# Kernel tuning notes

Measured on AMD Instinct MI355X. Metric: run time of the kernel, lower is better.

## Reference

```python
import jax, jax.numpy as jnp
import numpy as np

N, E = 50000, 1600000
IN_DIM, EMBED, OUT = 512, 128, 64


def setup_inputs() -> dict:
    key = jax.random.key(0)
    k = jax.random.split(key, 8)
    x = jax.random.normal(k[0], (N, IN_DIM), dtype=jnp.float32)
    edge_index = jax.random.randint(k[1], (2, E), 0, N, dtype=jnp.int32)
    W_dense = jax.random.normal(k[2], (EMBED, IN_DIM), dtype=jnp.float32) * 0.02
    b_dense = jnp.zeros((EMBED,), dtype=jnp.float32)
    W_gat = jax.random.normal(k[3], (OUT, EMBED), dtype=jnp.float32) * 0.05
    att_src = jax.random.normal(k[4], (OUT,), dtype=jnp.float32) * 0.1
    att_dst = jax.random.normal(k[5], (OUT,), dtype=jnp.float32) * 0.1
    b_gat = jnp.zeros((OUT,), dtype=jnp.float32)
    return {"x": x, "edge_index": edge_index, "W_dense": W_dense, "b_dense": b_dense,
            "W_gat": W_gat, "att_src": att_src, "att_dst": att_dst, "b_gat": b_gat}


def reference(x, edge_index, W_dense, b_dense, W_gat, att_src, att_dst, b_gat):
    # dense -> LeakyReLU(0.01) (nn.LeakyReLU default)
    h = jax.nn.leaky_relu(x @ W_dense.T + b_dense, negative_slope=0.01)  # [N, EMBED]
    n = h.shape[0]
    # GATConv (PyG, heads=1, add_self_loops=True, negative_slope=0.2)
    loops = jnp.arange(n, dtype=edge_index.dtype)
    src = jnp.concatenate([edge_index[0], loops])
    dst = jnp.concatenate([edge_index[1], loops])
    g = h @ W_gat.T  # [N, OUT]
    a_src = g @ att_src  # [N]
    a_dst = g @ att_dst  # [N]
    e = jax.nn.leaky_relu(a_src[src] + a_dst[dst], negative_slope=0.2)  # [E+N]
    # segment softmax over destination neighborhoods (self loops guarantee non-empty)
    m = jax.ops.segment_max(e, dst, num_segments=n)
    e = jnp.exp(e - m[dst])
    denom = jax.ops.segment_sum(e, dst, num_segments=n)
    alpha = e / denom[dst]
    out = jax.ops.segment_sum(g[src] * alpha[:, None], dst, num_segments=n) + b_gat
    # original returns ([embed_x], [embed_x]); we return the single embedding tensor
    return out
```

## Files before the change

kernel.cpp:

```cpp
#include <hip/hip_runtime.h>
#include <math.h>

#define IN_DIM 512
#define EMBED 128
#define OUT_DIM 64
#define NBPAD 256
#define SEGSH 12
#define CAP_LDS 10240

typedef __attribute__((ext_vector_type(8))) short bf16x8;
typedef __attribute__((ext_vector_type(4))) float f32x4;

__device__ __forceinline__ float lrelu(float v, float s) { return v > 0.f ? v : v * s; }

__device__ __forceinline__ float readlane_f(float v, int l) {
  return __int_as_float(__builtin_amdgcn_readlane(__float_as_int(v), l));
}

__device__ __forceinline__ unsigned short f2bf(float f) {
  unsigned int u = __float_as_uint(f);
  u += 0x7fff + ((u >> 16) & 1);
  return (unsigned short)(u >> 16);
}
__device__ __forceinline__ float bf2f(unsigned short h) {
  return __uint_as_float(((unsigned int)h) << 16);
}

__device__ __forceinline__ unsigned int cvt_pk_bf16(float a, float b) {
  unsigned int r;
  asm("v_cvt_pk_bf16_f32 %0, %1, %2" : "=v"(r) : "v"(a), "v"(b));
  return r;
}

__device__ __forceinline__ void gl_lds16(const void* g, void* l) {
  __builtin_amdgcn_global_load_lds(
      (const __attribute__((address_space(1))) unsigned int*)g,
      (__attribute__((address_space(3))) unsigned int*)l, 16, 0, 0);
}

#define LDA 40

__global__ __launch_bounds__(256) void split_w_kernel(
    const float* __restrict__ Wd, unsigned short* __restrict__ Wdh,
    unsigned short* __restrict__ Wdl, const float* __restrict__ Wg,
    unsigned short* __restrict__ Wgh, unsigned short* __restrict__ Wgl) {
  int i = (blockIdx.x * 256 + threadIdx.x) * 4;
  const float* W;
  unsigned short *Wh, *Wl;
  int base;
  if (i < EMBED * IN_DIM) {
    W = Wd; Wh = Wdh; Wl = Wdl; base = i;
  } else {
    base = i - EMBED * IN_DIM;
    if (base >= OUT_DIM * EMBED) return;
    W = Wg; Wh = Wgh; Wl = Wgl;
  }
  float4 v = *(const float4*)(W + base);
  unsigned int h0 = cvt_pk_bf16(v.x, v.y);
  unsigned int h1 = cvt_pk_bf16(v.z, v.w);
  float r0 = v.x - __uint_as_float(h0 << 16);
  float r1 = v.y - __uint_as_float(h0 & 0xffff0000u);
  float r2 = v.z - __uint_as_float(h1 << 16);
  float r3 = v.w - __uint_as_float(h1 & 0xffff0000u);
  unsigned int l0 = cvt_pk_bf16(r0, r1);
  unsigned int l1 = cvt_pk_bf16(r2, r3);
  *(uint2*)(Wh + base) = make_uint2(h0, h1);
  *(uint2*)(Wl + base) = make_uint2(l0, l1);
}

__global__ __launch_bounds__(256) void gemm1_mfma_kernel(
    const float* __restrict__ x, const unsigned short* __restrict__ Wdh,
    const unsigned short* __restrict__ Wdl, const float* __restrict__ bd,
    unsigned int* __restrict__ hp, int N) {
  __shared__ __align__(16) unsigned char Bhs[2][8192];
  __shared__ __align__(16) unsigned char Bls[2][8192];

  const int tid = threadIdx.x;
  const int lane = tid & 63;
  const int wid = tid >> 6;
  const int mblk = blockIdx.x * 128;
  const int quad = lane >> 4;
  const int l15 = lane & 15;

  const float* aptr[2];
#pragma unroll
  for (int mi = 0; mi < 2; ++mi) {
    int rg = mblk + wid * 32 + mi * 16 + l15;
    if (rg >= N) rg = N - 1;
    aptr[mi] = x + (size_t)rg * IN_DIM + quad * 8;
  }
  float4 tc[2][2];
  auto loadA = [&](int k0) {
#pragma unroll
    for (int mi = 0; mi < 2; ++mi) {
      tc[mi][0] = *(const float4*)(aptr[mi] + k0);
      tc[mi][1] = *(const float4*)(aptr[mi] + k0 + 4);
    }
  };

  const char* bsrcH[2];
  const char* bsrcL[2];
  int bdst[2];
#pragma unroll
  for (int i = 0; i < 2; ++i) {
    int chunk = i * 256 + tid;
    int row = chunk >> 2, ch = chunk & 3;
    int cs = ch ^ ((row >> 1) & 3);
    size_t srcoff = (size_t)row * (IN_DIM * 2) + (cs << 4);
    bsrcH[i] = (const char*)Wdh + srcoff;
    bsrcL[i] = (const char*)Wdl + srcoff;
    bdst[i] = chunk * 16;
  }
  auto stageB = [&](int buf, int k0) {
    const size_t kb = (size_t)k0 * 2;
#pragma unroll
    for (int i = 0; i < 2; ++i) {
      gl_lds16(bsrcH[i] + kb, Bhs[buf] + bdst[i]);
      gl_lds16(bsrcL[i] + kb, Bls[buf] + bdst[i]);
    }
  };

  int boff[8];
#pragma unroll
  for (int ni = 0; ni < 8; ++ni) {
    int row = ni * 16 + l15;
    boff[ni] = row * 64 + ((quad ^ ((row >> 1) & 3)) << 4);
  }

  f32x4 acc[2][8];
#pragma unroll
  for (int i = 0; i < 2; ++i)
#pragma unroll
    for (int j = 0; j < 8; ++j) acc[i][j] = (f32x4){0.f, 0.f, 0.f, 0.f};

  stageB(0, 0);
  loadA(0);
  __syncthreads();

#pragma unroll 2
  for (int s = 0; s < IN_DIM / 32; ++s) {
    const int buf = s & 1;
    if (s + 1 < IN_DIM / 32) stageB(buf ^ 1, (s + 1) * 32);

    bf16x8 AH[2], AL[2];
#pragma unroll
    for (int mi = 0; mi < 2; ++mi) {
      float av[8] = {tc[mi][0].x, tc[mi][0].y, tc[mi][0].z, tc[mi][0].w,
                     tc[mi][1].x, tc[mi][1].y, tc[mi][1].z, tc[mi][1].w};
      union { unsigned int u[4]; bf16x8 v; } H, L;
#pragma unroll
      for (int i = 0; i < 4; ++i) {
        unsigned int hpk = cvt_pk_bf16(av[2 * i], av[2 * i + 1]);
        float q0 = av[2 * i] - __uint_as_float(hpk << 16);
        float q1 = av[2 * i + 1] - __uint_as_float(hpk & 0xffff0000u);
        H.u[i] = hpk;
        L.u[i] = cvt_pk_bf16(q0, q1);
      }
      AH[mi] = H.v;
      AL[mi] = L.v;
    }
    if (s + 1 < IN_DIM / 32) loadA((s + 1) * 32);

#pragma unroll
    for (int hf = 0; hf < 2; ++hf) {
      bf16x8 BH[4], BL[4];
#pragma unroll
      for (int j = 0; j < 4; ++j) {
        BH[j] = *(const bf16x8*)(Bhs[buf] + boff[hf * 4 + j]);
        BL[j] = *(const bf16x8*)(Bls[buf] + boff[hf * 4 + j]);
      }
#pragma unroll
      for (int mi = 0; mi < 2; ++mi)
#pragma unroll
        for (int j = 0; j < 4; ++j) {
          int ni = hf * 4 + j;
          acc[mi][ni] = __builtin_amdgcn_mfma_f32_16x16x32_bf16(AH[mi], BH[j], acc[mi][ni], 0, 0, 0);
          acc[mi][ni] = __builtin_amdgcn_mfma_f32_16x16x32_bf16(AL[mi], BH[j], acc[mi][ni], 0, 0, 0);
          acc[mi][ni] = __builtin_amdgcn_mfma_f32_16x16x32_bf16(AH[mi], BL[j], acc[mi][ni], 0, 0, 0);
        }
    }
    __syncthreads();
  }

#pragma unroll
  for (int mi = 0; mi < 2; ++mi)
#pragma unroll
    for (int ni = 0; ni < 8; ++ni) {
      int n = ni * 16 + l15;
      float b = bd[n];
#pragma unroll
      for (int r = 0; r < 4; ++r) {
        int m = mblk + wid * 32 + mi * 16 + quad * 4 + r;
        float v = lrelu(acc[mi][ni][r] + b, 0.01f);
        unsigned short hi = f2bf(v);
        unsigned short lo = f2bf(v - bf2f(hi));
        if (m < N) hp[(size_t)m * EMBED + n] = ((unsigned int)hi << 16) | lo;
      }
    }
}

__global__ __launch_bounds__(256) void gemm2_mfma_kernel(
    const unsigned int* __restrict__ hp, const unsigned short* __restrict__ Wgh,
    const unsigned short* __restrict__ Wgl, const float* __restrict__ att_src,
    const float* __restrict__ att_dst, float* __restrict__ g,
    float* __restrict__ a_src, float* __restrict__ a_dst, int N) {
  __shared__ __align__(16) unsigned char Bhs[16384];
  __shared__ __align__(16) unsigned char Bls[16384];

  const int tid = threadIdx.x;
  const int lane = tid & 63;
  const int wid = tid >> 6;
  const int mblk = blockIdx.x * 128;
  const int quad = lane >> 4;
  const int l15 = lane & 15;

  const char* aptr[2];
#pragma unroll
  for (int mi = 0; mi < 2; ++mi) {
    int rg = mblk + wid * 32 + mi * 16 + l15;
    if (rg >= N) rg = N - 1;
    aptr[mi] = (const char*)hp + (size_t)rg * (EMBED * 4) + quad * 32;
  }
  uint4 areg[2][4][2];
#pragma unroll
  for (int mi = 0; mi < 2; ++mi)
#pragma unroll
    for (int ks = 0; ks < 4; ++ks) {
      areg[mi][ks][0] = *(const uint4*)(aptr[mi] + ks * 128);
      areg[mi][ks][1] = *(const uint4*)(aptr[mi] + ks * 128 + 16);
    }

#pragma unroll
  for (int i = 0; i < 4; ++i) {
    int chunk = i * 256 + tid;
    int row = chunk >> 4, ch = chunk & 15;
    size_t srcoff = (size_t)row * (EMBED * 2) + ((ch ^ (row & 15)) << 4);
    gl_lds16((const char*)Wgh + srcoff, Bhs + chunk * 16);
    gl_lds16((const char*)Wgl + srcoff, Bls + chunk * 16);
  }
  __syncthreads();

  f32x4 acc[2][4];
#pragma unroll
  for (int i = 0; i < 2; ++i)
#pragma unroll
    for (int j = 0; j < 4; ++j) acc[i][j] = (f32x4){0.f, 0.f, 0.f, 0.f};

#pragma unroll
  for (int ks = 0; ks < 4; ++ks) {
    bf16x8 AH[2], AL[2];
#pragma unroll
    for (int mi = 0; mi < 2; ++mi) {
      union { unsigned int u[8]; uint4 v[2]; } W_;
      W_.v[0] = areg[mi][ks][0];
      W_.v[1] = areg[mi][ks][1];
      union { unsigned int u[4]; bf16x8 v; } H, L;
#pragma unroll
      for (int p = 0; p < 4; ++p) {
        unsigned int wA = W_.u[2 * p], wB = W_.u[2 * p + 1];
        H.u[p] = __builtin_amdgcn_perm(wB, wA, 0x07060302u);
        L.u[p] = __builtin_amdgcn_perm(wB, wA, 0x05040100u);
      }
      AH[mi] = H.v;
      AL[mi] = L.v;
    }
#pragma unroll
    for (int ni = 0; ni < 4; ++ni) {
      int row = ni * 16 + l15;
      int chunk = ks * 4 + quad;
      int off = row * 256 + (((chunk ^ (row & 15))) << 4);
      bf16x8 BH = *(const bf16x8*)(Bhs + off);
      bf16x8 BL = *(const bf16x8*)(Bls + off);
#pragma unroll
      for (int mi = 0; mi < 2; ++mi) {
        acc[mi][ni] = __builtin_amdgcn_mfma_f32_16x16x32_bf16(AH[mi], BH, acc[mi][ni], 0, 0, 0);
        acc[mi][ni] = __builtin_amdgcn_mfma_f32_16x16x32_bf16(AL[mi], BH, acc[mi][ni], 0, 0, 0);
        acc[mi][ni] = __builtin_amdgcn_mfma_f32_16x16x32_bf16(AH[mi], BL, acc[mi][ni], 0, 0, 0);
      }
    }
  }

  float as_[4], ad_[4];
#pragma unroll
  for (int ni = 0; ni < 4; ++ni) {
    int n = ni * 16 + l15;
    as_[ni] = att_src[n];
    ad_[ni] = att_dst[n];
  }
#pragma unroll
  for (int mi = 0; mi < 2; ++mi) {
#pragma unroll
    for (int r = 0; r < 4; ++r) {
      int m = mblk + wid * 32 + mi * 16 + quad * 4 + r;
      float ps = acc[mi][0][r] * as_[0] + acc[mi][1][r] * as_[1] +
                 acc[mi][2][r] * as_[2] + acc[mi][3][r] * as_[3];
      float pd = acc[mi][0][r] * ad_[0] + acc[mi][1][r] * ad_[1] +
                 acc[mi][2][r] * ad_[2] + acc[mi][3][r] * ad_[3];
#pragma unroll
      for (int d = 1; d < 16; d <<= 1) {
        ps += __shfl_xor(ps, d, 64);
        pd += __shfl_xor(pd, d, 64);
      }
      if (m < N) {
#pragma unroll
        for (int ni = 0; ni < 4; ++ni)
          g[(size_t)m * OUT_DIM + ni * 16 + l15] = acc[mi][ni][r];
        if (l15 == 0) {
          a_src[m] = ps;
          a_dst[m] = pd;
        }
      }
    }
  }
}

__global__ __launch_bounds__(256) void hist_count_kernel(
    const int* __restrict__ ei, int* __restrict__ histT, int nblkP, int E,
    int N) {
  __shared__ int cnt[NBPAD];
  const int t = threadIdx.x;
  cnt[t] = 0;
  __syncthreads();
  const int T = E + N;
  const int base = blockIdx.x << SEGSH;
#pragma unroll
  for (int q = 0; q < (1 << SEGSH) / 256; ++q) {
    int i = base + q * 256 + t;
    if (i < T) {
      int d = (i < E) ? ei[E + i] : (i - E);
      atomicAdd(&cnt[d >> 8], 1);
    }
  }
  __syncthreads();
  histT[(size_t)t * nblkP + blockIdx.x] = cnt[t];
}

__global__ __launch_bounds__(256) void row_scan_kernel(
    int* __restrict__ histT, int* __restrict__ bucket_tot, int nblkP) {
  __shared__ int sc[256];
  const int t = threadIdx.x;
  int* row = histT + (size_t)blockIdx.x * nblkP;
  const int per = (nblkP + 255) / 256;
  int loc[8];
  int sum = 0;
#pragma unroll 4
  for (int j = 0; j < per; ++j) {
    int idx = t * per + j;
    int v = (idx < nblkP) ? row[idx] : 0;
    loc[j] = sum;
    sum += v;
  }
  sc[t] = sum;
  __syncthreads();
  for (int dlt = 1; dlt < 256; dlt <<= 1) {
    int add = (t >= dlt) ? sc[t - dlt] : 0;
    __syncthreads();
    sc[t] += add;
    __syncthreads();
  }
  const int off = sc[t] - sum;
#pragma unroll 4
  for (int j = 0; j < per; ++j) {
    int idx = t * per + j;
    if (idx < nblkP) row[idx] = off + loc[j];
  }
  if (t == 255) bucket_tot[blockIdx.x] = sc[255];
}

__global__ __launch_bounds__(256) void base_scan_kernel(
    const int* __restrict__ bucket_tot, int* __restrict__ bucket_base,
    int* __restrict__ offsets, int N, int T) {
  __shared__ int sc[256];
  const int t = threadIdx.x;
  int v = bucket_tot[t];
  sc[t] = v;
  __syncthreads();
  for (int dlt = 1; dlt < 256; dlt <<= 1) {
    int add = (t >= dlt) ? sc[t - dlt] : 0;
    __syncthreads();
    sc[t] += add;
    __syncthreads();
  }
  bucket_base[t] = sc[t] - v;
  if (t == 0) offsets[N] = T;
}

__global__ __launch_bounds__(256) void bin_kernel(
    const int* __restrict__ ei, const int* __restrict__ histT,
    const int* __restrict__ bucket_base, int* __restrict__ stageB, int nblkP,
    int E, int N) {
  __shared__ int cnt[NBPAD];
  __shared__ int basev[NBPAD];
  const int t = threadIdx.x;
  cnt[t] = 0;
  basev[t] = bucket_base[t] + histT[(size_t)t * nblkP + blockIdx.x];
  __syncthreads();
  const int T = E + N;
  const int base = blockIdx.x << SEGSH;
#pragma unroll
  for (int q = 0; q < (1 << SEGSH) / 256; ++q) {
    int i = base + q * 256 + t;
    if (i < T) {
      int s, d;
      if (i < E) {
        s = ei[i];
        d = ei[E + i];
      } else {
        s = d = i - E;
      }
      int b = d >> 8;
      int r = atomicAdd(&cnt[b], 1);
      stageB[basev[b] + r] = (s << 8) | (d & 255);
    }
  }
}

__global__ __launch_bounds__(256) void build_kernel(
    const int* __restrict__ stageB, const int* __restrict__ bucket_base,
    const int* __restrict__ bucket_tot, const float* __restrict__ a_src,
    const float* __restrict__ a_dst, int* __restrict__ offsets,
    int2* __restrict__ csr_pack, int N) {
  __shared__ int cnt[256];
  __shared__ int pre[256];
  __shared__ int cur[256];
  __shared__ int2 buf[CAP_LDS];
  const int b = blockIdx.x;
  const int t = threadIdx.x;
  const int base = bucket_base[b];
  const int tot = bucket_tot[b];
  cnt[t] = 0;
  __syncthreads();
  const int* sp = stageB + base;
  for (int i = t; i < tot; i += 256) atomicAdd(&cnt[sp[i] & 255], 1);
  __syncthreads();
  int v = cnt[t];
  pre[t] = v;
  __syncthreads();
  for (int dlt = 1; dlt < 256; dlt <<= 1) {
    int add = (t >= dlt) ? pre[t - dlt] : 0;
    __syncthreads();
    pre[t] += add;
    __syncthreads();
  }
  const int excl = pre[t] - v;
  cur[t] = excl;
  const int d_self = (b << 8) | t;
  if (d_self < N) offsets[d_self] = base + excl;
  __syncthreads();
  for (int i = t; i < tot; i += 256) {
    int rec = sp[i];
    int dl = rec & 255;
    int s = rec >> 8;
    float e = a_src[s] + a_dst[(b << 8) | dl];
    e = e > 0.f ? e : 0.2f * e;
    int pos = atomicAdd(&cur[dl], 1);
    int2 r2 = make_int2(s, __float_as_int(e));
    if (pos < CAP_LDS)
      buf[pos] = r2;
    else
      csr_pack[base + pos] = r2;
  }
  __syncthreads();
  const int lim = min(tot, CAP_LDS);
  for (int i = t; i < lim; i += 256) csr_pack[base + i] = buf[i];
}

__global__ __launch_bounds__(256) void aggregate_kernel(
    const int* __restrict__ offsets, const int2* __restrict__ csr_pack,
    const float* __restrict__ g, const float* __restrict__ b_gat,
    float* __restrict__ out, int N) {
  const int lane = threadIdx.x & 63;
  const int node = blockIdx.x * 4 + (threadIdx.x >> 6);
  if (node >= N) return;
  const int beg = offsets[node], end = offsets[node + 1];

  float m = -1e30f;
  for (int j = beg + lane; j < end; j += 64)
    m = fmaxf(m, __int_as_float(csr_pack[j].y));
#pragma unroll
  for (int d = 1; d < 64; d <<= 1) m = fmaxf(m, __shfl_xor(m, d, 64));

  float l = 0.f;
  for (int j = beg + lane; j < end; j += 64)
    l += __expf(__int_as_float(csr_pack[j].y) - m);
#pragma unroll
  for (int d = 1; d < 64; d <<= 1) l += __shfl_xor(l, d, 64);
  const float inv_l = 1.f / l;

  float acc0 = 0.f, acc1 = 0.f, acc2 = 0.f, acc3 = 0.f;
  for (int jb = beg; jb < end; jb += 64) {
    int j = jb + lane;
    float p = 0.f;
    int s = 0;
    if (j < end) {
      int2 rec = csr_pack[j];
      p = __expf(__int_as_float(rec.y) - m) * inv_l;
      s = rec.x;
    }
    const int cnt = min(64, end - jb);
    int jj = 0;
    for (; jj + 4 <= cnt; jj += 4) {
      int s0 = __builtin_amdgcn_readlane(s, jj);
      int s1 = __builtin_amdgcn_readlane(s, jj + 1);
      int s2 = __builtin_amdgcn_readlane(s, jj + 2);
      int s3 = __builtin_amdgcn_readlane(s, jj + 3);
      float p0 = readlane_f(p, jj);
      float p1 = readlane_f(p, jj + 1);
      float p2 = readlane_f(p, jj + 2);
      float p3 = readlane_f(p, jj + 3);
      acc0 += p0 * g[((size_t)s0 << 6) + lane];
      acc1 += p1 * g[((size_t)s1 << 6) + lane];
      acc2 += p2 * g[((size_t)s2 << 6) + lane];
      acc3 += p3 * g[((size_t)s3 << 6) + lane];
    }
    for (; jj < cnt; ++jj) {
      int s0 = __builtin_amdgcn_readlane(s, jj);
      float p0 = readlane_f(p, jj);
      acc0 += p0 * g[((size_t)s0 << 6) + lane];
    }
  }
  out[(size_t)node * OUT_DIM + lane] = (acc0 + acc1) + (acc2 + acc3) + b_gat[lane];
}

extern "C" void kernel_launch(void* const* d_in, const int* in_sizes, int n_in,
                              void* d_out, int out_size, void* d_ws, size_t ws_size,
                              hipStream_t stream) {
  const float* x = (const float*)d_in[0];
  const int* ei = (const int*)d_in[1];
  const float* Wd = (const float*)d_in[2];
  const float* bd = (const float*)d_in[3];
  const float* Wg = (const float*)d_in[4];
  const float* att_src = (const float*)d_in[5];
  const float* att_dst = (const float*)d_in[6];
  const float* bg = (const float*)d_in[7];
  float* out = (float*)d_out;

  const int N = in_sizes[0] / IN_DIM;
  const int E = in_sizes[1] / 2;
  const int T = E + N;
  const int NB = (N + 255) >> 8;
  const int nblkP = (T + (1 << SEGSH) - 1) >> SEGSH;

  char* ws = (char*)d_ws;
  size_t off = 0;
  auto alloc = [&](size_t bytes) -> void* {
    void* p = ws + off;
    off += (bytes + 15) & ~(size_t)15;
    return p;
  };
  unsigned int* hpk = (unsigned int*)alloc((size_t)N * EMBED * 4);
  float* g = (float*)alloc((size_t)N * OUT_DIM * 4);
  float* a_src = (float*)alloc((size_t)N * 4);
  float* a_dst = (float*)alloc((size_t)N * 4);
  int* offsets = (int*)alloc((size_t)(N + 1) * 4);
  int* histT = (int*)alloc((size_t)NBPAD * nblkP * 4);
  int* bucket_base = (int*)alloc((size_t)NBPAD * 4);
  int* bucket_tot = (int*)alloc((size_t)NBPAD * 4);
  int* stageB = (int*)alloc((size_t)T * 4);
  int2* csr_pack = (int2*)alloc((size_t)T * 8);
  unsigned short* Wdh = (unsigned short*)alloc((size_t)EMBED * IN_DIM * 2);
  unsigned short* Wdl = (unsigned short*)alloc((size_t)EMBED * IN_DIM * 2);
  unsigned short* Wgh = (unsigned short*)alloc((size_t)OUT_DIM * EMBED * 2);
  unsigned short* Wgl = (unsigned short*)alloc((size_t)OUT_DIM * EMBED * 2);

  const int SPLIT_TOT = EMBED * IN_DIM + OUT_DIM * EMBED;
  hipLaunchKernelGGL(split_w_kernel, dim3(SPLIT_TOT / 1024), dim3(256), 0,
                     stream, Wd, Wdh, Wdl, Wg, Wgh, Wgl);
  hipLaunchKernelGGL(gemm1_mfma_kernel, dim3((N + 127) / 128), dim3(256), 0,
                     stream, x, Wdh, Wdl, bd, hpk, N);
  hipLaunchKernelGGL(gemm2_mfma_kernel, dim3((N + 127) / 128), dim3(256), 0,
                     stream, hpk, Wgh, Wgl, att_src, att_dst, g, a_src, a_dst, N);
  hipLaunchKernelGGL(hist_count_kernel, dim3(nblkP), dim3(256), 0, stream,
                     ei, histT, nblkP, E, N);
  hipLaunchKernelGGL(row_scan_kernel, dim3(NBPAD), dim3(256), 0, stream,
                     histT, bucket_tot, nblkP);
  hipLaunchKernelGGL(base_scan_kernel, dim3(1), dim3(256), 0, stream,
                     bucket_tot, bucket_base, offsets, N, T);
  hipLaunchKernelGGL(bin_kernel, dim3(nblkP), dim3(256), 0, stream,
                     ei, histT, bucket_base, stageB, nblkP, E, N);
  hipLaunchKernelGGL(build_kernel, dim3(NB), dim3(256), 0, stream,
                     stageB, bucket_base, bucket_tot, a_src, a_dst, offsets,
                     csr_pack, N);
  hipLaunchKernelGGL(aggregate_kernel, dim3((N + 3) / 4), dim3(256), 0, stream,
                     offsets, csr_pack, g, bg, out, N);
}
```

Measured before the change: 316.6 us.

## Use 512-thread blocks in gemm1 and single-pass online softmax in aggregate

The first GEMM now runs 8 waves per block, each handling 16 rows instead of 32. This halves per-thread accumulators and A registers, and spreads the B staging over more threads, for more latency hiding and occupancy. The aggregate kernel merges the max pass and the sum-of-exp pass into one online-softmax pass with a combined (max, sum) wave reduction, so csr_pack is read one time fewer. The cost is extra exp calls in the loop and reduction, and less MFMA work per wave to amortise each LDS read of B.

```diff
diff --git a/kernel.cpp b/kernel.cpp
--- a/kernel.cpp
+++ b/kernel.cpp
@@ -37,8 +37,6 @@
       (const __attribute__((address_space(1))) unsigned int*)g,
       (__attribute__((address_space(3))) unsigned int*)l, 16, 0, 0);
 }
-
-#define LDA 40
 
 __global__ __launch_bounds__(256) void split_w_kernel(
     const float* __restrict__ Wd, unsigned short* __restrict__ Wdh,
@@ -68,7 +66,7 @@
   *(uint2*)(Wl + base) = make_uint2(l0, l1);
 }
 
-__global__ __launch_bounds__(256) void gemm1_mfma_kernel(
+__global__ __launch_bounds__(512) void gemm1_mfma_kernel(
     const float* __restrict__ x, const unsigned short* __restrict__ Wdh,
     const unsigned short* __restrict__ Wdl, const float* __restrict__ bd,
     unsigned int* __restrict__ hp, int N) {
@@ -82,42 +80,31 @@
   const int quad = lane >> 4;
   const int l15 = lane & 15;
 
-  const float* aptr[2];
-#pragma unroll
-  for (int mi = 0; mi < 2; ++mi) {
-    int rg = mblk + wid * 32 + mi * 16 + l15;
-    if (rg >= N) rg = N - 1;
-    aptr[mi] = x + (size_t)rg * IN_DIM + quad * 8;
-  }
-  float4 tc[2][2];
+  int rg = mblk + wid * 16 + l15;
+  if (rg >= N) rg = N - 1;
+  const float* aptr = x + (size_t)rg * IN_DIM + quad * 8;
+  float4 tc0, tc1;
   auto loadA = [&](int k0) {
-#pragma unroll
-    for (int mi = 0; mi < 2; ++mi) {
-      tc[mi][0] = *(const float4*)(aptr[mi] + k0);
-      tc[mi][1] = *(const float4*)(aptr[mi] + k0 + 4);
-    }
+    tc0 = *(const float4*)(aptr + k0);
+    tc1 = *(const float4*)(aptr + k0 + 4);
   };
 
-  const char* bsrcH[2];
-  const char* bsrcL[2];
-  int bdst[2];
-#pragma unroll
-  for (int i = 0; i < 2; ++i) {
-    int chunk = i * 256 + tid;
+  const char* bsrcH;
+  const char* bsrcL;
+  int bdstv;
+  {
+    int chunk = tid;
     int row = chunk >> 2, ch = chunk & 3;
     int cs = ch ^ ((row >> 1) & 3);
     size_t srcoff = (size_t)row * (IN_DIM * 2) + (cs << 4);
-    bsrcH[i] = (const char*)Wdh + srcoff;
-    bsrcL[i] = (const char*)Wdl + srcoff;
-    bdst[i] = chunk * 16;
+    bsrcH = (const char*)Wdh + srcoff;
+    bsrcL = (const char*)Wdl + srcoff;
+    bdstv = chunk * 16;
   }
   auto stageB = [&](int buf, int k0) {
     const size_t kb = (size_t)k0 * 2;
-#pragma unroll
-    for (int i = 0; i < 2; ++i) {
-      gl_lds16(bsrcH[i] + kb, Bhs[buf] + bdst[i]);
-      gl_lds16(bsrcL[i] + kb, Bls[buf] + bdst[i]);
-    }
+    gl_lds16(bsrcH + kb, Bhs[buf] + bdstv);
+    gl_lds16(bsrcL + kb, Bls[buf] + bdstv);
   };
 
   int boff[8];
@@ -127,11 +114,9 @@
     boff[ni] = row * 64 + ((quad ^ ((row >> 1) & 3)) << 4);
   }
 
-  f32x4 acc[2][8];
-#pragma unroll
-  for (int i = 0; i < 2; ++i)
-#pragma unroll
-    for (int j = 0; j < 8; ++j) acc[i][j] = (f32x4){0.f, 0.f, 0.f, 0.f};
+  f32x4 acc[8];
+#pragma unroll
+  for (int j = 0; j < 8; ++j) acc[j] = (f32x4){0.f, 0.f, 0.f, 0.f};
 
   stageB(0, 0);
   loadA(0);
@@ -142,11 +127,9 @@
     const int buf = s & 1;
     if (s + 1 < IN_DIM / 32) stageB(buf ^ 1, (s + 1) * 32);
 
-    bf16x8 AH[2], AL[2];
-#pragma unroll
-    for (int mi = 0; mi < 2; ++mi) {
-      float av[8] = {tc[mi][0].x, tc[mi][0].y, tc[mi][0].z, tc[mi][0].w,
-                     tc[mi][1].x, tc[mi][1].y, tc[mi][1].z, tc[mi][1].w};
+    bf16x8 AH, AL;
+    {
+      float av[8] = {tc0.x, tc0.y, tc0.z, tc0.w, tc1.x, tc1.y, tc1.z, tc1.w};
       union { unsigned int u[4]; bf16x8 v; } H, L;
 #pragma unroll
       for (int i = 0; i < 4; ++i) {
@@ -156,8 +139,8 @@
         H.u[i] = hpk;
         L.u[i] = cvt_pk_bf16(q0, q1);
       }
-      AH[mi] = H.v;
-      AL[mi] = L.v;
+      AH = H.v;
+      AL = L.v;
     }
     if (s + 1 < IN_DIM / 32) loadA((s + 1) * 32);
 
@@ -170,33 +153,29 @@
         BL[j] = *(const bf16x8*)(Bls[buf] + boff[hf * 4 + j]);
       }
 #pragma unroll
-      for (int mi = 0; mi < 2; ++mi)
-#pragma unroll
-        for (int j = 0; j < 4; ++j) {
-          int ni = hf * 4 + j;
-          acc[mi][ni] = __builtin_amdgcn_mfma_f32_16x16x32_bf16(AH[mi], BH[j], acc[mi][ni], 0, 0, 0);
-          acc[mi][ni] = __builtin_amdgcn_mfma_f32_16x16x32_bf16(AL[mi], BH[j], acc[mi][ni], 0, 0, 0);
-          acc[mi][ni] = __builtin_amdgcn_mfma_f32_16x16x32_bf16(AH[mi], BL[j], acc[mi][ni], 0, 0, 0);
-        }
-    }
-    __syncthreads();
-  }
-
-#pragma unroll
-  for (int mi = 0; mi < 2; ++mi)
-#pragma unroll
-    for (int ni = 0; ni < 8; ++ni) {
-      int n = ni * 16 + l15;
-      float b = bd[n];
-#pragma unroll
-      for (int r = 0; r < 4; ++r) {
-        int m = mblk + wid * 32 + mi * 16 + quad * 4 + r;
-        float v = lrelu(acc[mi][ni][r] + b, 0.01f);
-        unsigned short hi = f2bf(v);
-        unsigned short lo = f2bf(v - bf2f(hi));
-        if (m < N) hp[(size_t)m * EMBED + n] = ((unsigned int)hi << 16) | lo;
-      }
-    }
+      for (int j = 0; j < 4; ++j) {
+        int ni = hf * 4 + j;
+        acc[ni] = __builtin_amdgcn_mfma_f32_16x16x32_bf16(AH, BH[j], acc[ni], 0, 0, 0);
+        acc[ni] = __builtin_amdgcn_mfma_f32_16x16x32_bf16(AL, BH[j], acc[ni], 0, 0, 0);
+        acc[ni] = __builtin_amdgcn_mfma_f32_16x16x32_bf16(AH, BL[j], acc[ni], 0, 0, 0);
+      }
+    }
+    __syncthreads();
+  }
+
+#pragma unroll
+  for (int ni = 0; ni < 8; ++ni) {
+    int n = ni * 16 + l15;
+    float b = bd[n];
+#pragma unroll
+    for (int r = 0; r < 4; ++r) {
+      int m = mblk + wid * 16 + quad * 4 + r;
+      float v = lrelu(acc[ni][r] + b, 0.01f);
+      unsigned short hi = f2bf(v);
+      unsigned short lo = f2bf(v - bf2f(hi));
+      if (m < N) hp[(size_t)m * EMBED + n] = ((unsigned int)hi << 16) | lo;
+    }
+  }
 }
 
 __global__ __launch_bounds__(256) void gemm2_mfma_kernel(
@@ -474,17 +453,24 @@
   if (node >= N) return;
   const int beg = offsets[node], end = offsets[node + 1];
 
-  float m = -1e30f;
-  for (int j = beg + lane; j < end; j += 64)
-    m = fmaxf(m, __int_as_float(csr_pack[j].y));
-#pragma unroll
-  for (int d = 1; d < 64; d <<= 1) m = fmaxf(m, __shfl_xor(m, d, 64));
-
-  float l = 0.f;
-  for (int j = beg + lane; j < end; j += 64)
-    l += __expf(__int_as_float(csr_pack[j].y) - m);
-#pragma unroll
-  for (int d = 1; d < 64; d <<= 1) l += __shfl_xor(l, d, 64);
+  float m = -1e30f, l = 0.f;
+  for (int j = beg + lane; j < end; j += 64) {
+    float e = __int_as_float(csr_pack[j].y);
+    if (e > m) {
+      l = l * __expf(m - e) + 1.f;
+      m = e;
+    } else {
+      l += __expf(e - m);
+    }
+  }
+#pragma unroll
+  for (int d = 1; d < 64; d <<= 1) {
+    float mo = __shfl_xor(m, d, 64);
+    float lo = __shfl_xor(l, d, 64);
+    float M = fmaxf(m, mo);
+    l = l * __expf(m - M) + lo * __expf(mo - M);
+    m = M;
+  }
   const float inv_l = 1.f / l;
 
   float acc0 = 0.f, acc1 = 0.f, acc2 = 0.f, acc3 = 0.f;
@@ -566,7 +552,7 @@
   const int SPLIT_TOT = EMBED * IN_DIM + OUT_DIM * EMBED;
   hipLaunchKernelGGL(split_w_kernel, dim3(SPLIT_TOT / 1024), dim3(256), 0,
                      stream, Wd, Wdh, Wdl, Wg, Wgh, Wgl);
-  hipLaunchKernelGGL(gemm1_mfma_kernel, dim3((N + 127) / 128), dim3(256), 0,
+  hipLaunchKernelGGL(gemm1_mfma_kernel, dim3((N + 127) / 128), dim3(512), 0,
                      stream, x, Wdh, Wdl, bd, hpk, N);
   hipLaunchKernelGGL(gemm2_mfma_kernel, dim3((N + 127) / 128), dim3(256), 0,
                      stream, hpk, Wgh, Wgl, att_src, att_dst, g, a_src, a_dst, N);
```

New measurement: 318.4 us. Within noise of the previous version (+0.6%).

## Store GAT features in fp16 and fuse softmax max/sum into online pass

Applied to the files above, without the earlier changes.

The projected features g are now written as fp16 instead of fp32, halving the bytes gathered per edge in the aggregation kernel, which is dominated by random row reads. The separate max and sum passes over each node's edge list become a single online-softmax pass that combines (max, sum) pairs across lanes. This trades precision in g (fp16 rounding) for bandwidth, and adds extra exp evaluations in the online rescaling and the cross-lane reduction.

```diff
diff --git a/kernel.cpp b/kernel.cpp
--- a/kernel.cpp
+++ b/kernel.cpp
@@ -1,4 +1,5 @@
 #include <hip/hip_runtime.h>
+#include <hip/hip_fp16.h>
 #include <math.h>
 
 #define IN_DIM 512
@@ -37,8 +38,6 @@
       (const __attribute__((address_space(1))) unsigned int*)g,
       (__attribute__((address_space(3))) unsigned int*)l, 16, 0, 0);
 }
-
-#define LDA 40
 
 __global__ __launch_bounds__(256) void split_w_kernel(
     const float* __restrict__ Wd, unsigned short* __restrict__ Wdh,
@@ -202,7 +201,7 @@
 __global__ __launch_bounds__(256) void gemm2_mfma_kernel(
     const unsigned int* __restrict__ hp, const unsigned short* __restrict__ Wgh,
     const unsigned short* __restrict__ Wgl, const float* __restrict__ att_src,
-    const float* __restrict__ att_dst, float* __restrict__ g,
+    const float* __restrict__ att_dst, __half* __restrict__ gh,
     float* __restrict__ a_src, float* __restrict__ a_dst, int N) {
   __shared__ __align__(16) unsigned char Bhs[16384];
   __shared__ __align__(16) unsigned char Bls[16384];
@@ -304,7 +303,7 @@
       if (m < N) {
 #pragma unroll
         for (int ni = 0; ni < 4; ++ni)
-          g[(size_t)m * OUT_DIM + ni * 16 + l15] = acc[mi][ni][r];
+          gh[(size_t)m * OUT_DIM + ni * 16 + l15] = __float2half(acc[mi][ni][r]);
         if (l15 == 0) {
           a_src[m] = ps;
           a_dst[m] = pd;
@@ -467,24 +466,31 @@
 
 __global__ __launch_bounds__(256) void aggregate_kernel(
     const int* __restrict__ offsets, const int2* __restrict__ csr_pack,
-    const float* __restrict__ g, const float* __restrict__ b_gat,
+    const __half* __restrict__ gh, const float* __restrict__ b_gat,
     float* __restrict__ out, int N) {
   const int lane = threadIdx.x & 63;
   const int node = blockIdx.x * 4 + (threadIdx.x >> 6);
   if (node >= N) return;
   const int beg = offsets[node], end = offsets[node + 1];
 
-  float m = -1e30f;
-  for (int j = beg + lane; j < end; j += 64)
-    m = fmaxf(m, __int_as_float(csr_pack[j].y));
-#pragma unroll
-  for (int d = 1; d < 64; d <<= 1) m = fmaxf(m, __shfl_xor(m, d, 64));
-
-  float l = 0.f;
-  for (int j = beg + lane; j < end; j += 64)
-    l += __expf(__int_as_float(csr_pack[j].y) - m);
-#pragma unroll
-  for (int d = 1; d < 64; d <<= 1) l += __shfl_xor(l, d, 64);
+  float m = -1e30f, l = 0.f;
+  for (int j = beg + lane; j < end; j += 64) {
+    float e = __int_as_float(csr_pack[j].y);
+    if (e > m) {
+      l = l * __expf(m - e) + 1.f;
+      m = e;
+    } else {
+      l += __expf(e - m);
+    }
+  }
+#pragma unroll
+  for (int d = 1; d < 64; d <<= 1) {
+    float mo = __shfl_xor(m, d, 64);
+    float lo = __shfl_xor(l, d, 64);
+    float M = fmaxf(m, mo);
+    l = l * __expf(m - M) + lo * __expf(mo - M);
+    m = M;
+  }
   const float inv_l = 1.f / l;
 
   float acc0 = 0.f, acc1 = 0.f, acc2 = 0.f, acc3 = 0.f;
@@ -508,15 +514,15 @@
       float p1 = readlane_f(p, jj + 1);
       float p2 = readlane_f(p, jj + 2);
       float p3 = readlane_f(p, jj + 3);
-      acc0 += p0 * g[((size_t)s0 << 6) + lane];
-      acc1 += p1 * g[((size_t)s1 << 6) + lane];
-      acc2 += p2 * g[((size_t)s2 << 6) + lane];
-      acc3 += p3 * g[((size_t)s3 << 6) + lane];
+      acc0 += p0 * __half2float(gh[((size_t)s0 << 6) + lane]);
+      acc1 += p1 * __half2float(gh[((size_t)s1 << 6) + lane]);
+      acc2 += p2 * __half2float(gh[((size_t)s2 << 6) + lane]);
+      acc3 += p3 * __half2float(gh[((size_t)s3 << 6) + lane]);
     }
     for (; jj < cnt; ++jj) {
       int s0 = __builtin_amdgcn_readlane(s, jj);
       float p0 = readlane_f(p, jj);
-      acc0 += p0 * g[((size_t)s0 << 6) + lane];
+      acc0 += p0 * __half2float(gh[((size_t)s0 << 6) + lane]);
     }
   }
   out[(size_t)node * OUT_DIM + lane] = (acc0 + acc1) + (acc2 + acc3) + b_gat[lane];
@@ -549,7 +555,7 @@
     return p;
   };
   unsigned int* hpk = (unsigned int*)alloc((size_t)N * EMBED * 4);
-  float* g = (float*)alloc((size_t)N * OUT_DIM * 4);
+  __half* gh = (__half*)alloc((size_t)N * OUT_DIM * 2);
   float* a_src = (float*)alloc((size_t)N * 4);
   float* a_dst = (float*)alloc((size_t)N * 4);
   int* offsets = (int*)alloc((size_t)(N + 1) * 4);
@@ -569,7 +575,7 @@
   hipLaunchKernelGGL(gemm1_mfma_kernel, dim3((N + 127) / 128), dim3(256), 0,
                      stream, x, Wdh, Wdl, bd, hpk, N);
   hipLaunchKernelGGL(gemm2_mfma_kernel, dim3((N + 127) / 128), dim3(256), 0,
-                     stream, hpk, Wgh, Wgl, att_src, att_dst, g, a_src, a_dst, N);
+                     stream, hpk, Wgh, Wgl, att_src, att_dst, gh, a_src, a_dst, N);
   hipLaunchKernelGGL(hist_count_kernel, dim3(nblkP), dim3(256), 0, stream,
                      ei, histT, nblkP, E, N);
   hipLaunchKernelGGL(row_scan_kernel, dim3(NBPAD), dim3(256), 0, stream,
@@ -582,5 +588,5 @@
                      stageB, bucket_base, bucket_tot, a_src, a_dst, offsets,
                      csr_pack, N);
   hipLaunchKernelGGL(aggregate_kernel, dim3((N + 3) / 4), dim3(256), 0, stream,
-                     offsets, csr_pack, g, bg, out, N);
-}
+                     offsets, csr_pack, gh, bg, out, N);
+}
```

Result: faster. 306.2 us (-3.3%).
